# Performance work log

Hardware: AMD Instinct MI355X
Metric: run time of the kernel (lower is better)

The kernel has to match this reference:

```python
import jax, jax.numpy as jnp
import numpy as np

B, D, O = 8192, 64, 256

def setup_inputs() -> dict:
    key = jax.random.key(0)
    k1, k2, k3 = jax.random.split(key, 3)
    x = jax.random.normal(k1, (B, D), dtype=jnp.float32)
    centers = jax.random.uniform(k2, (O, 1, D), dtype=jnp.float32)  # RandomUniform(0,1)
    # Original uses Constant(10.0) which saturates exp(-quad) to 0; use small random
    # betas so the quadratic form is in a numerically meaningful range.
    betas = jax.random.normal(k3, (O, D, D), dtype=jnp.float32) * 0.05
    return {"x": x, "centers": centers, "betas": betas}

def reference(x, centers, betas):
    # precision[o] = betas[o] @ betas[o]^T   -> [O, D, D]
    precision = jnp.einsum('ode,ofe->odf', betas, betas)
    # diff[o,b,:] = centers[o] - x[b]        -> [O, B, D]
    diff = centers - x[None, :, :]
    # quad[o,b] = diff[o,b]^T P[o] diff[o,b] -> [O, B]
    quad = jnp.einsum('obd,odf,obf->ob', diff, precision, diff)
    return jnp.exp(-quad).T  # [B, O]
```

## Files before the change

kernel.cpp:

```cpp
#include <hip/hip_runtime.h>
#include <hip/hip_bf16.h>

typedef __bf16 bf16x8 __attribute__((ext_vector_type(8)));
typedef float  f32x4  __attribute__((ext_vector_type(4)));
typedef float  f32x16 __attribute__((ext_vector_type(16)));

constexpr int Bn = 8192, Dn = 64, On = 256;

#define GLD16(g, l) __builtin_amdgcn_global_load_lds( \
    (const __attribute__((address_space(1))) void*)(g), \
    (__attribute__((address_space(3))) void*)(l), 16, 0, 0)
#define GLD4(g, l) __builtin_amdgcn_global_load_lds( \
    (const __attribute__((address_space(1))) void*)(g), \
    (__attribute__((address_space(3))) void*)(l), 4, 0, 0)

__global__ void k_prep(const float* __restrict__ betas, const float* __restrict__ centers,
                       __bf16* __restrict__ bTsw, float* __restrict__ ncpk) {
    __shared__ float s[64 * 65];
    const int o = blockIdx.x, tid = threadIdx.x;
    const float* bo = betas + (size_t)o * 4096;
    for (int j = tid; j < 1024; j += 256) {
        int d = j >> 4, e4 = (j & 15) * 4;
        float4 v = ((const float4*)bo)[j];
        s[d * 65 + e4 + 0] = v.x; s[d * 65 + e4 + 1] = v.y;
        s[d * 65 + e4 + 2] = v.z; s[d * 65 + e4 + 3] = v.w;
    }
    __syncthreads();
    for (int j = tid; j < 4096; j += 256) {
        int e = j >> 6, dpos = j & 63;
        int slot = dpos >> 3, jj = dpos & 7;
        int d = ((slot ^ (e & 7)) << 3) + jj;
        bTsw[(size_t)o * 4096 + j] = (__bf16)s[d * 65 + e];
    }
    if (tid < 64) {
        int et = tid >> 5, rem = tid & 31, l5 = rem >> 4, reg = rem & 15;
        int row = et * 32 + l5 * 4 + (reg & 3) + ((reg >> 2) << 3);
        float acc = 0.f;
        for (int d = 0; d < 64; ++d) acc += s[d * 65 + row] * centers[o * 64 + d];
        ncpk[o * 64 + tid] = -acc;
    }
}

__global__ void __launch_bounds__(256)
__attribute__((amdgpu_waves_per_eu(2, 2)))
k_main(const float* __restrict__ x, const __bf16* __restrict__ bTsw,
       const float* __restrict__ ncpk, float* __restrict__ out) {
    __shared__ __align__(16) __bf16 sX[128 * 64];
    __shared__ __align__(16) __bf16 sA[4][64 * 64];
    __shared__ __align__(16) float  sCp[4][64];

    const int tid = threadIdx.x, wq = tid >> 6, lane = tid & 63;
    const int l31 = lane & 31, l5 = lane >> 5;
    const int bbase = blockIdx.x * 128;
    const int o0 = blockIdx.y * 32 + wq * 8;

#pragma unroll
    for (int i = 0; i < 4; ++i) {
        int id = i * 256 + tid, rb = id >> 3, c = id & 7;
        const float* xp = x + (size_t)(bbase + rb) * 64 + c * 8;
        float4 v0 = *(const float4*)xp, v1 = *(const float4*)(xp + 4);
        bf16x8 f;
        f[0] = (__bf16)v0.x; f[1] = (__bf16)v0.y; f[2] = (__bf16)v0.z; f[3] = (__bf16)v0.w;
        f[4] = (__bf16)v1.x; f[5] = (__bf16)v1.y; f[6] = (__bf16)v1.z; f[7] = (__bf16)v1.w;
        *(bf16x8*)(sX + rb * 64 + ((c ^ (rb & 7)) << 3)) = f;
    }
    __syncthreads();

    bf16x8 xf[4][4];
#pragma unroll
    for (int bt = 0; bt < 4; ++bt)
#pragma unroll
        for (int k = 0; k < 4; ++k) {
            int row = bt * 32 + l31, c = k * 2 + l5;
            xf[bt][k] = *(const bf16x8*)(sX + row * 64 + ((c ^ (row & 7)) << 3));
        }

    __bf16* myA  = &sA[wq][0];
    float*  myCp = &sCp[wq][0];

    for (int oi = 0; oi < 8; ++oi) {
        const int o = o0 + oi;
        const __bf16* gA = bTsw + (size_t)o * 4096 + lane * 8;
#pragma unroll
        for (int cll = 0; cll < 8; ++cll)
            GLD16(gA + cll * 512, myA + cll * 512);
        GLD4(ncpk + o * 64 + lane, myCp);
        __builtin_amdgcn_sched_barrier(0);
        __builtin_amdgcn_s_waitcnt(0x0f70);
        __builtin_amdgcn_sched_barrier(0);

        f32x4 qv[4] = {{0.f,0.f,0.f,0.f},{0.f,0.f,0.f,0.f},{0.f,0.f,0.f,0.f},{0.f,0.f,0.f,0.f}};
#pragma unroll
        for (int et = 0; et < 2; ++et) {
            f32x16 cpv;
#pragma unroll
            for (int r4 = 0; r4 < 4; ++r4)
                ((f32x4*)&cpv)[r4] = *(const f32x4*)(myCp + et * 32 + l5 * 16 + r4 * 4);
            bf16x8 af[4];
#pragma unroll
            for (int k = 0; k < 4; ++k) {
                int row = et * 32 + l31, c = k * 2 + l5;
                af[k] = *(const bf16x8*)(myA + row * 64 + ((c ^ (row & 7)) << 3));
            }
#pragma unroll
            for (int bt = 0; bt < 4; ++bt) {
                f32x16 acc = __builtin_amdgcn_mfma_f32_32x32x16_bf16(af[0], xf[bt][0], cpv, 0, 0, 0);
                acc = __builtin_amdgcn_mfma_f32_32x32x16_bf16(af[1], xf[bt][1], acc, 0, 0, 0);
                acc = __builtin_amdgcn_mfma_f32_32x32x16_bf16(af[2], xf[bt][2], acc, 0, 0, 0);
                acc = __builtin_amdgcn_mfma_f32_32x32x16_bf16(af[3], xf[bt][3], acc, 0, 0, 0);
#pragma unroll
                for (int j = 0; j < 16; ++j)
                    qv[bt][j & 3] = fmaf(acc[j], acc[j], qv[bt][j & 3]);
            }
        }
        float q[4];
#pragma unroll
        for (int bt = 0; bt < 4; ++bt) {
            float qs = (qv[bt][0] + qv[bt][1]) + (qv[bt][2] + qv[bt][3]);
            qs += __shfl_xor(qs, 32, 64);
            q[bt] = qs;
        }
        float qA = l5 ? q[2] : q[0], qB = l5 ? q[3] : q[1];
        int bA = bbase + l5 * 64 + l31;
        out[(size_t)bA * 256 + o]        = __expf(-qA);
        out[(size_t)(bA + 32) * 256 + o] = __expf(-qB);
        __builtin_amdgcn_sched_barrier(0);
    }
}

extern "C" void kernel_launch(void* const* d_in, const int* in_sizes, int n_in,
                              void* d_out, int out_size, void* d_ws, size_t ws_size,
                              hipStream_t stream) {
    const float* x       = (const float*)d_in[0];
    const float* centers = (const float*)d_in[1];
    const float* betas   = (const float*)d_in[2];
    float* out = (float*)d_out;

    char* ws = (char*)d_ws;
    __bf16* bTsw = (__bf16*)ws;
    float*  ncpk = (float*)(ws + 2 * (1 << 20));

    k_prep<<<dim3(On),           dim3(256), 0, stream>>>(betas, centers, bTsw, ncpk);
    k_main<<<dim3(Bn / 128, On / 32), dim3(256), 0, stream>>>(x, bTsw, ncpk, out);
}
```

Before: 86.36 us.

## Share A tiles across waves with double-buffered prefetch and coalesced output stores

The block tiling changes so that all four waves share the same 8 outputs (o) and each wave handles its own 128 rows of x, loaded straight into registers. The per-o betas tile is loaded cooperatively by the block into a double-buffered LDS slot, so the next o is prefetched during compute. The bf16 layout is pre-permuted in the prep kernel so fragment loads are linear. Results pass through an LDS transpose so each row writes 8 contiguous floats instead of scattered 4-byte stores. The cost is a block-wide barrier on every o iteration and direct uncoalesced-ish global loads of x into registers.

```diff
diff --git a/kernel.cpp b/kernel.cpp
--- a/kernel.cpp
+++ b/kernel.cpp
@@ -10,9 +10,6 @@
 #define GLD16(g, l) __builtin_amdgcn_global_load_lds( \
     (const __attribute__((address_space(1))) void*)(g), \
     (__attribute__((address_space(3))) void*)(l), 16, 0, 0)
-#define GLD4(g, l) __builtin_amdgcn_global_load_lds( \
-    (const __attribute__((address_space(1))) void*)(g), \
-    (__attribute__((address_space(3))) void*)(l), 4, 0, 0)
 
 __global__ void k_prep(const float* __restrict__ betas, const float* __restrict__ centers,
                        __bf16* __restrict__ bTsw, float* __restrict__ ncpk) {
@@ -26,11 +23,12 @@
         s[d * 65 + e4 + 2] = v.z; s[d * 65 + e4 + 3] = v.w;
     }
     __syncthreads();
-    for (int j = tid; j < 4096; j += 256) {
-        int e = j >> 6, dpos = j & 63;
-        int slot = dpos >> 3, jj = dpos & 7;
-        int d = ((slot ^ (e & 7)) << 3) + jj;
-        bTsw[(size_t)o * 4096 + j] = (__bf16)s[d * 65 + e];
+    for (int p = tid; p < 4096; p += 256) {
+        int chunk = p >> 3, j = p & 7;
+        int ek = chunk >> 6, lane = chunk & 63;
+        int e = (ek >> 2) * 32 + (lane & 31);
+        int d = ((ek & 3) * 2 + (lane >> 5)) * 8 + j;
+        bTsw[(size_t)o * 4096 + p] = (__bf16)s[d * 65 + e];
     }
     if (tid < 64) {
         int et = tid >> 5, rem = tid & 31, l5 = rem >> 4, reg = rem & 15;
@@ -45,72 +43,71 @@
 __attribute__((amdgpu_waves_per_eu(2, 2)))
 k_main(const float* __restrict__ x, const __bf16* __restrict__ bTsw,
        const float* __restrict__ ncpk, float* __restrict__ out) {
-    __shared__ __align__(16) __bf16 sX[128 * 64];
-    __shared__ __align__(16) __bf16 sA[4][64 * 64];
-    __shared__ __align__(16) float  sCp[4][64];
+    __shared__ __align__(16) unsigned char smem[2 * 8192 + 2048];
+    __bf16* sA0 = (__bf16*)smem;
+    __bf16* sA1 = (__bf16*)(smem + 8192);
+    float*  sCp = (float*)(smem + 16384);
 
     const int tid = threadIdx.x, wq = tid >> 6, lane = tid & 63;
     const int l31 = lane & 31, l5 = lane >> 5;
-    const int bbase = blockIdx.x * 128;
-    const int o0 = blockIdx.y * 32 + wq * 8;
+    const int bbase = blockIdx.x * 512;
+    const int o0 = blockIdx.y * 8;
 
-#pragma unroll
-    for (int i = 0; i < 4; ++i) {
-        int id = i * 256 + tid, rb = id >> 3, c = id & 7;
-        const float* xp = x + (size_t)(bbase + rb) * 64 + c * 8;
-        float4 v0 = *(const float4*)xp, v1 = *(const float4*)(xp + 4);
-        bf16x8 f;
-        f[0] = (__bf16)v0.x; f[1] = (__bf16)v0.y; f[2] = (__bf16)v0.z; f[3] = (__bf16)v0.w;
-        f[4] = (__bf16)v1.x; f[5] = (__bf16)v1.y; f[6] = (__bf16)v1.z; f[7] = (__bf16)v1.w;
-        *(bf16x8*)(sX + rb * 64 + ((c ^ (rb & 7)) << 3)) = f;
-    }
-    __syncthreads();
+    sCp[tid]       = ncpk[o0 * 64 + tid];
+    sCp[256 + tid] = ncpk[o0 * 64 + 256 + tid];
 
     bf16x8 xf[4][4];
 #pragma unroll
     for (int bt = 0; bt < 4; ++bt)
 #pragma unroll
-        for (int k = 0; k < 4; ++k) {
-            int row = bt * 32 + l31, c = k * 2 + l5;
-            xf[bt][k] = *(const bf16x8*)(sX + row * 64 + ((c ^ (row & 7)) << 3));
+        for (int kk = 0; kk < 4; ++kk) {
+            const float* xp = x + (size_t)(bbase + wq * 128 + bt * 32 + l31) * 64
+                                + (kk * 2 + l5) * 8;
+            float4 v0 = *(const float4*)xp, v1 = *(const float4*)(xp + 4);
+            bf16x8 f;
+            f[0] = (__bf16)v0.x; f[1] = (__bf16)v0.y; f[2] = (__bf16)v0.z; f[3] = (__bf16)v0.w;
+            f[4] = (__bf16)v1.x; f[5] = (__bf16)v1.y; f[6] = (__bf16)v1.z; f[7] = (__bf16)v1.w;
+            xf[bt][kk] = f;
         }
 
-    __bf16* myA  = &sA[wq][0];
-    float*  myCp = &sCp[wq][0];
+    auto prefetch = [&](int o, __bf16* buf) {
+        const __bf16* g = bTsw + (size_t)o * 4096;
+        GLD16(g + (size_t)(wq * 128 + lane) * 8,      buf + (wq * 128) * 8);
+        GLD16(g + (size_t)(wq * 128 + 64 + lane) * 8, buf + (wq * 128 + 64) * 8);
+    };
 
+    float qd[16];
+    prefetch(o0, sA0);
+    __builtin_amdgcn_s_waitcnt(0x0f70);
+    __syncthreads();
+
+#pragma unroll
     for (int oi = 0; oi < 8; ++oi) {
-        const int o = o0 + oi;
-        const __bf16* gA = bTsw + (size_t)o * 4096 + lane * 8;
-#pragma unroll
-        for (int cll = 0; cll < 8; ++cll)
-            GLD16(gA + cll * 512, myA + cll * 512);
-        GLD4(ncpk + o * 64 + lane, myCp);
-        __builtin_amdgcn_sched_barrier(0);
-        __builtin_amdgcn_s_waitcnt(0x0f70);
-        __builtin_amdgcn_sched_barrier(0);
+        __bf16* cur = (oi & 1) ? sA1 : sA0;
+        if (oi < 7) prefetch(o0 + oi + 1, (oi & 1) ? sA0 : sA1);
 
-        f32x4 qv[4] = {{0.f,0.f,0.f,0.f},{0.f,0.f,0.f,0.f},{0.f,0.f,0.f,0.f},{0.f,0.f,0.f,0.f}};
+        f32x4 qv[4] = {{0,0,0,0},{0,0,0,0},{0,0,0,0},{0,0,0,0}};
 #pragma unroll
         for (int et = 0; et < 2; ++et) {
             f32x16 cpv;
 #pragma unroll
             for (int r4 = 0; r4 < 4; ++r4)
-                ((f32x4*)&cpv)[r4] = *(const f32x4*)(myCp + et * 32 + l5 * 16 + r4 * 4);
+                ((f32x4*)&cpv)[r4] = *(const f32x4*)(sCp + oi * 64 + et * 32 + l5 * 16 + r4 * 4);
             bf16x8 af[4];
 #pragma unroll
-            for (int k = 0; k < 4; ++k) {
-                int row = et * 32 + l31, c = k * 2 + l5;
-                af[k] = *(const bf16x8*)(myA + row * 64 + ((c ^ (row & 7)) << 3));
-            }
+            for (int k = 0; k < 4; ++k)
+                af[k] = *(const bf16x8*)(cur + (size_t)((et * 4 + k) * 64 + lane) * 8);
 #pragma unroll
             for (int bt = 0; bt < 4; ++bt) {
                 f32x16 acc = __builtin_amdgcn_mfma_f32_32x32x16_bf16(af[0], xf[bt][0], cpv, 0, 0, 0);
                 acc = __builtin_amdgcn_mfma_f32_32x32x16_bf16(af[1], xf[bt][1], acc, 0, 0, 0);
                 acc = __builtin_amdgcn_mfma_f32_32x32x16_bf16(af[2], xf[bt][2], acc, 0, 0, 0);
                 acc = __builtin_amdgcn_mfma_f32_32x32x16_bf16(af[3], xf[bt][3], acc, 0, 0, 0);
-#pragma unroll
-                for (int j = 0; j < 16; ++j)
-                    qv[bt][j & 3] = fmaf(acc[j], acc[j], qv[bt][j & 3]);
+                const f32x4* aq = (const f32x4*)&acc;
+                qv[bt] += aq[0] * aq[0];
+                qv[bt] += aq[1] * aq[1];
+                qv[bt] += aq[2] * aq[2];
+                qv[bt] += aq[3] * aq[3];
             }
         }
         float q[4];
@@ -120,11 +117,31 @@
             qs += __shfl_xor(qs, 32, 64);
             q[bt] = qs;
         }
-        float qA = l5 ? q[2] : q[0], qB = l5 ? q[3] : q[1];
-        int bA = bbase + l5 * 64 + l31;
-        out[(size_t)bA * 256 + o]        = __expf(-qA);
-        out[(size_t)(bA + 32) * 256 + o] = __expf(-qB);
+        qd[oi * 2 + 0] = l5 ? q[2] : q[0];
+        qd[oi * 2 + 1] = l5 ? q[3] : q[1];
+
         __builtin_amdgcn_sched_barrier(0);
+        __builtin_amdgcn_s_waitcnt(0x0f70);
+        __syncthreads();
+    }
+
+    float* scr = (float*)smem + wq * 1152;
+#pragma unroll
+    for (int oi = 0; oi < 8; ++oi) {
+        scr[(l5 * 64 + l31) * 9 + oi]      = qd[oi * 2 + 0];
+        scr[(l5 * 64 + 32 + l31) * 9 + oi] = qd[oi * 2 + 1];
+    }
+    __syncthreads();
+#pragma unroll
+    for (int rr = 0; rr < 2; ++rr) {
+        int r = lane * 2 + rr;
+        const float* q8 = scr + r * 9;
+        f32x4 r0, r1;
+#pragma unroll
+        for (int j = 0; j < 4; ++j) { r0[j] = __expf(-q8[j]); r1[j] = __expf(-q8[4 + j]); }
+        float* op = out + (size_t)(bbase + wq * 128 + r) * 256 + o0;
+        *(f32x4*)op       = r0;
+        *(f32x4*)(op + 4) = r1;
     }
 }
 
@@ -140,6 +157,6 @@
     __bf16* bTsw = (__bf16*)ws;
     float*  ncpk = (float*)(ws + 2 * (1 << 20));
 
-    k_prep<<<dim3(On),           dim3(256), 0, stream>>>(betas, centers, bTsw, ncpk);
-    k_main<<<dim3(Bn / 128, On / 32), dim3(256), 0, stream>>>(x, bTsw, ncpk, out);
+    k_prep<<<dim3(On),                dim3(256), 0, stream>>>(betas, centers, bTsw, ncpk);
+    k_main<<<dim3(Bn / 512, On / 8),  dim3(256), 0, stream>>>(x, bTsw, ncpk, out);
 }
```

Measured after the change: 87.52 us. Within noise of the previous version (+1.3%).
